# Performance work log

Measured on AMD Instinct MI355X. Metric: run time of the kernel, lower is better.

## Reference

```python
import jax, jax.numpy as jnp
import numpy as np

N, E = 50000, 800000
IN_C, HID_C, OUT_C, HEADS = 128, 32, 16, 4
NEG_SLOPE = 0.2


def gat_conv(x, src, dst, W, att_src, att_dst, bias, heads, out_ch, concat, n_nodes):
    # linear transform: [N, heads, out_ch]
    h = (x @ W).reshape(n_nodes, heads, out_ch)
    # per-node attention logits [N, heads]
    a_s = (h * att_src).sum(-1)
    a_d = (h * att_dst).sum(-1)
    # per-edge raw attention (edge j->i uses src logit of j, dst logit of i)
    alpha = jax.nn.leaky_relu(a_s[src] + a_d[dst], negative_slope=NEG_SLOPE)  # [E, heads]
    # segment softmax over destination neighborhoods
    amax = jax.ops.segment_max(alpha, dst, num_segments=n_nodes)
    ex = jnp.exp(alpha - amax[dst])
    den = jax.ops.segment_sum(ex, dst, num_segments=n_nodes)
    coef = ex / den[dst]  # [E, heads]
    # weighted scatter-add aggregation
    msg = h[src] * coef[:, :, None]  # [E, heads, out_ch]
    out = jax.ops.segment_sum(msg, dst, num_segments=n_nodes)  # [N, heads, out_ch]
    out = out.reshape(n_nodes, heads * out_ch) if concat else out.mean(axis=1)
    return out + bias


def setup_inputs() -> dict:
    key = jax.random.key(0)
    ks = jax.random.split(key, 10)
    x = jax.random.normal(ks[0], (N, IN_C), dtype=jnp.float32)
    edge_index = jax.random.randint(ks[1], (2, E), 0, N, dtype=jnp.int64)
    s1 = 1.0 / np.sqrt(IN_C)
    s2 = 1.0 / np.sqrt(HID_C * HEADS)
    W1 = jax.random.normal(ks[2], (IN_C, HEADS * HID_C), dtype=jnp.float32) * s1
    att_src1 = jax.random.normal(ks[3], (HEADS, HID_C), dtype=jnp.float32) * s1
    att_dst1 = jax.random.normal(ks[4], (HEADS, HID_C), dtype=jnp.float32) * s1
    b1 = jnp.zeros((HEADS * HID_C,), dtype=jnp.float32)
    W2 = jax.random.normal(ks[5], (HEADS * HID_C, OUT_C), dtype=jnp.float32) * s2
    att_src2 = jax.random.normal(ks[6], (1, OUT_C), dtype=jnp.float32) * s2
    att_dst2 = jax.random.normal(ks[7], (1, OUT_C), dtype=jnp.float32) * s2
    b2 = jnp.zeros((OUT_C,), dtype=jnp.float32)
    return {"x": x, "edge_index": edge_index, "W1": W1, "att_src1": att_src1,
            "att_dst1": att_dst1, "b1": b1, "W2": W2, "att_src2": att_src2,
            "att_dst2": att_dst2, "b2": b2}


def reference(x, edge_index, W1, att_src1, att_dst1, b1, W2, att_src2, att_dst2, b2):
    n = x.shape[0]
    # PyG GATConv default: add self loops
    ar = jnp.arange(n, dtype=edge_index.dtype)
    src = jnp.concatenate([edge_index[0], ar])
    dst = jnp.concatenate([edge_index[1], ar])
    h = gat_conv(x, src, dst, W1, att_src1, att_dst1, b1, HEADS, HID_C, True, n)
    h = jax.nn.elu(h)
    out = gat_conv(h, src, dst, W2, att_src2, att_dst2, b2, 1, OUT_C, False, n)
    return out
```

## Files before the change

### kernel.cpp

```cpp
#include <hip/hip_runtime.h>

typedef __attribute__((ext_vector_type(8))) short short8;
typedef __attribute__((ext_vector_type(4))) float f32x4;

__device__ __forceinline__ float lrelu02(float a) { return a > 0.0f ? a : 0.2f * a; }

__device__ __forceinline__ unsigned bf16rne(float f) {
    unsigned u = __float_as_uint(f);
    return (u + 0x7fffu + ((u >> 16) & 1u)) >> 16;
}

__global__ __launch_bounds__(256) void k_zero(int4* __restrict__ p, int n4) {
    int i = blockIdx.x * blockDim.x + threadIdx.x;
    if (i < n4) p[i] = make_int4(0, 0, 0, 0);
}

__global__ __launch_bounds__(256) void k_g1rank(
    const float* __restrict__ x, const float* __restrict__ W,
    const float* __restrict__ attS, const float* __restrict__ attD,
    unsigned short* __restrict__ h1, float* __restrict__ as1, float* __restrict__ ad1,
    const int* __restrict__ ei, int* __restrict__ deg, int* __restrict__ rank,
    int E, int N, int RB)
{
    __shared__ unsigned short Wt[128 * 128];
    __shared__ unsigned short xs[64 * 128];

    if (blockIdx.x < RB) {
        int tid = blockIdx.x * blockDim.x + threadIdx.x;
        int nthr = RB * blockDim.x;
        int E4 = E & ~3;
        for (int b = tid * 4; b < E4; b += nthr * 4) {
            int4 d = *(const int4*)(ei + E + b);
            int4 r;
            r.x = atomicAdd(&deg[d.x], 1);
            r.y = atomicAdd(&deg[d.y], 1);
            r.z = atomicAdd(&deg[d.z], 1);
            r.w = atomicAdd(&deg[d.w], 1);
            *(int4*)(rank + b) = r;
        }
        for (int e = E4 + tid; e < E; e += nthr)
            rank[e] = atomicAdd(&deg[ei[E + e]], 1);
        for (int i = tid; i < N; i += nthr)
            rank[E + i] = atomicAdd(&deg[i], 1);
        return;
    }

    const int t = threadIdx.x;
    const int lane = t & 63;
    const int wv = t >> 6;
    const int ln = lane & 15;
    const int lg = lane >> 4;
    const int r0 = (blockIdx.x - RB) * 64;

    #pragma unroll
    for (int i = 0; i < 16; ++i) {
        int flat = i * 256 + t;
        int n = flat & 127;
        int k0 = (flat >> 7) * 4;
        float v0 = W[(size_t)(k0 + 0) * 128 + n];
        float v1 = W[(size_t)(k0 + 1) * 128 + n];
        float v2 = W[(size_t)(k0 + 2) * 128 + n];
        float v3 = W[(size_t)(k0 + 3) * 128 + n];
        uint2 pk;
        pk.x = bf16rne(v0) | (bf16rne(v1) << 16);
        pk.y = bf16rne(v2) | (bf16rne(v3) << 16);
        int byteo = n * 256 + ((k0 * 2) ^ ((n & 7) << 4));
        *(uint2*)((char*)Wt + byteo) = pk;
    }
    {
        int mbase = t >> 5, k0 = (t & 31) * 4;
        #pragma unroll
        for (int it = 0; it < 8; ++it) {
            int m = mbase + it * 8;
            int rr = r0 + m;
            float4 v = make_float4(0.f, 0.f, 0.f, 0.f);
            if (rr < N) v = *(const float4*)&x[(size_t)rr * 128 + k0];
            unsigned lo = bf16rne(v.x) | (bf16rne(v.y) << 16);
            unsigned hi = bf16rne(v.z) | (bf16rne(v.w) << 16);
            int byteo = m * 256 + ((k0 * 2) ^ ((m & 7) << 4));
            *(uint2*)((char*)xs + byteo) = make_uint2(lo, hi);
        }
    }
    __syncthreads();

    f32x4 acc[8];
    #pragma unroll
    for (int i = 0; i < 8; ++i) acc[i] = (f32x4)(0.f);

    #pragma unroll
    for (int kk = 0; kk < 4; ++kk) {
        int kb = (kk * 32 + lg * 8) * 2;
        int am = wv * 16 + ln;
        short8 a = *(const short8*)((char*)xs + am * 256 + (kb ^ ((am & 7) << 4)));
        #pragma unroll
        for (int tile = 0; tile < 8; ++tile) {
            int n = tile * 16 + ln;
            short8 b = *(const short8*)((char*)Wt + n * 256 + (kb ^ ((n & 7) << 4)));
            acc[tile] = __builtin_amdgcn_mfma_f32_16x16x32_bf16(a, b, acc[tile], 0, 0, 0);
        }
    }

    float aSt[8], aDt[8];
    #pragma unroll
    for (int tile = 0; tile < 8; ++tile) {
        aSt[tile] = attS[tile * 16 + ln];
        aDt[tile] = attD[tile * 16 + ln];
    }
    #pragma unroll
    for (int r = 0; r < 4; ++r) {
        int row = r0 + wv * 16 + lg * 4 + r;
        #pragma unroll
        for (int h = 0; h < 4; ++h) {
            float s = acc[2*h][r] * aSt[2*h] + acc[2*h+1][r] * aSt[2*h+1];
            float d = acc[2*h][r] * aDt[2*h] + acc[2*h+1][r] * aDt[2*h+1];
            s += __shfl_xor(s, 1); s += __shfl_xor(s, 2); s += __shfl_xor(s, 4); s += __shfl_xor(s, 8);
            d += __shfl_xor(d, 1); d += __shfl_xor(d, 2); d += __shfl_xor(d, 4); d += __shfl_xor(d, 8);
            if (ln == h * 4 + r && row < N) {
                as1[row * 4 + h] = s;
                ad1[row * 4 + h] = d;
            }
        }
    }

    __syncthreads();
    #pragma unroll
    for (int tile = 0; tile < 8; ++tile) {
        #pragma unroll
        for (int r = 0; r < 4; ++r) {
            int m = wv * 16 + lg * 4 + r;
            int byteo = m * 256 + (((tile * 16 + ln) * 2) ^ ((m & 7) << 4));
            *(unsigned short*)((char*)xs + byteo) = (unsigned short)bf16rne(acc[tile][r]);
        }
    }
    __syncthreads();
    #pragma unroll
    for (int it = 0; it < 4; ++it) {
        int idx = t + it * 256;
        int m = idx >> 4, o = idx & 15;
        int byteo = m * 256 + ((o * 16) ^ ((m & 7) << 4));
        if (r0 + m < N)
            *(uint4*)((char*)(h1 + (size_t)(r0 + m) * 128) + o * 16) =
                *(const uint4*)((const char*)xs + byteo);
    }
}

__global__ __launch_bounds__(256) void k_scan_local(
    const int* __restrict__ deg, int* __restrict__ rowptr, int* __restrict__ bsum, int N)
{
    const int t = threadIdx.x;
    const int base = blockIdx.x * 2048 + t * 8;
    int v[8];
    int s = 0;
    #pragma unroll
    for (int j = 0; j < 8; ++j) {
        int idx = base + j;
        v[j] = (idx < N) ? deg[idx] : 0;
        s += v[j];
    }
    __shared__ int ts[256];
    ts[t] = s;
    __syncthreads();
    #pragma unroll
    for (int off = 1; off < 256; off <<= 1) {
        int u = (t >= off) ? ts[t - off] : 0;
        __syncthreads();
        ts[t] += u;
        __syncthreads();
    }
    int ex = (t == 0) ? 0 : ts[t - 1];
    #pragma unroll
    for (int j = 0; j < 8; ++j) {
        int idx = base + j;
        if (idx < N) rowptr[idx] = ex;
        ex += v[j];
    }
    if (t == 255) bsum[blockIdx.x] = ts[255];
}

__global__ __launch_bounds__(256) void k_scan_add(
    int* __restrict__ rowptr, const int* __restrict__ bsum, int N, int ET)
{
    const int t = threadIdx.x;
    __shared__ int soff;
    if (t < 64) {
        int v = (t < (int)blockIdx.x) ? bsum[t] : 0;
        #pragma unroll
        for (int m = 32; m >= 1; m >>= 1) v += __shfl_xor(v, m);
        if (t == 0) soff = v;
    }
    __syncthreads();
    int off = soff;
    const int base = blockIdx.x * 2048 + t * 8;
    #pragma unroll
    for (int j = 0; j < 8; ++j) {
        int idx = base + j;
        if (idx < N) rowptr[idx] += off;
    }
    if (blockIdx.x == 0 && t == 0) rowptr[N] = ET;
}

__global__ __launch_bounds__(256) void k_fill2(const int* __restrict__ ei,
                                               const int* __restrict__ rank,
                                               const int* __restrict__ rowptr,
                                               int* __restrict__ col, int E, int N) {
    int tid = blockIdx.x * blockDim.x + threadIdx.x;
    int nthr = gridDim.x * blockDim.x;
    int E4 = E & ~3;
    for (int b = tid * 4; b < E4; b += nthr * 4) {
        int4 d = *(const int4*)(ei + E + b);
        int4 s = *(const int4*)(ei + b);
        int4 r = *(const int4*)(rank + b);
        col[rowptr[d.x] + r.x] = s.x;
        col[rowptr[d.y] + r.y] = s.y;
        col[rowptr[d.z] + r.z] = s.z;
        col[rowptr[d.w] + r.w] = s.w;
    }
    for (int e = E4 + tid; e < E; e += nthr)
        col[rowptr[ei[E + e]] + rank[e]] = ei[e];
    for (int i = tid; i < N; i += nthr)
        col[rowptr[i] + rank[E + i]] = i;
}

__global__ __launch_bounds__(256) void k_agg1(
    const unsigned short* __restrict__ h1, const float* __restrict__ as1,
    const float* __restrict__ ad1, const int* __restrict__ rowptr,
    const int* __restrict__ col, const float* __restrict__ b1,
    unsigned short* __restrict__ out1, int N)
{
    int wid = (int)(((unsigned)blockIdx.x * blockDim.x + threadIdx.x) >> 6);
    if (wid >= N) return;
    int lane = threadIdx.x & 63;
    int start = rowptr[wid], end = rowptr[wid + 1];
    const float4 ad = *(const float4*)(ad1 + (size_t)wid * 4);

    float den0 = 0.f, den1 = 0.f, den2 = 0.f, den3 = 0.f;
    for (int e = start + lane; e < end; e += 64) {
        int src = col[e];
        const float4 a = *(const float4*)(as1 + (size_t)src * 4);
        den0 += __expf(lrelu02(a.x + ad.x));
        den1 += __expf(lrelu02(a.y + ad.y));
        den2 += __expf(lrelu02(a.z + ad.z));
        den3 += __expf(lrelu02(a.w + ad.w));
    }
    #pragma unroll
    for (int m = 32; m >= 1; m >>= 1) {
        den0 += __shfl_xor(den0, m); den1 += __shfl_xor(den1, m);
        den2 += __shfl_xor(den2, m); den3 += __shfl_xor(den3, m);
    }
    int head = lane >> 4;
    float rden = head == 0 ? 1.f/den0 : head == 1 ? 1.f/den1 : head == 2 ? 1.f/den2 : 1.f/den3;
    float adh  = head == 0 ? ad.x : head == 1 ? ad.y : head == 2 ? ad.z : ad.w;

    float acc0 = 0.f, acc1 = 0.f;
    for (int e = start; e < end; e += 8) {
        int s[8];
        float av[8], km[8];
        unsigned hv[8];
        #pragma unroll
        for (int j = 0; j < 8; ++j) {
            int ee = e + j;
            bool ok = ee < end;
            int es = ok ? ee : e;
            s[j]  = col[es];
            km[j] = ok ? 1.f : 0.f;
        }
        #pragma unroll
        for (int j = 0; j < 8; ++j)
            av[j] = as1[(size_t)s[j] * 4 + head];
        #pragma unroll
        for (int j = 0; j < 8; ++j)
            hv[j] = *(const unsigned*)(h1 + (size_t)s[j] * 128 + lane * 2);
        #pragma unroll
        for (int j = 0; j < 8; ++j) {
            float coef = km[j] * __expf(lrelu02(av[j] + adh)) * rden;
            acc0 = fmaf(coef, __uint_as_float(hv[j] << 16), acc0);
            acc1 = fmaf(coef, __uint_as_float(hv[j] & 0xffff0000u), acc1);
        }
    }
    int c0 = lane * 2;
    float o0 = acc0 + b1[c0];
    float o1 = acc1 + b1[c0 + 1];
    o0 = o0 > 0.f ? o0 : expm1f(o0);
    o1 = o1 > 0.f ? o1 : expm1f(o1);
    unsigned ov = bf16rne(o0) | (bf16rne(o1) << 16);
    *(unsigned*)((char*)out1 + (size_t)wid * 256 + lane * 4) = ov;
}

__global__ __launch_bounds__(256) void k_gemm2(
    const unsigned short* __restrict__ in, const float* __restrict__ W,
    const float* __restrict__ attS, const float* __restrict__ attD,
    float* __restrict__ h2, float* __restrict__ as2, float* __restrict__ ad2, int N)
{
    __shared__ unsigned short Wt[16 * 128];
    __shared__ unsigned short xs[64 * 128];
    const int t = threadIdx.x;
    const int lane = t & 63;
    const int wv = t >> 6;
    const int ln = lane & 15;
    const int lg = lane >> 4;
    const int r0 = blockIdx.x * 64;

    #pragma unroll
    for (int i = 0; i < 2; ++i) {
        int flat = i * 256 + t;
        int n = flat & 15;
        int k0 = (flat >> 4) * 4;
        float v0 = W[(size_t)(k0 + 0) * 16 + n];
        float v1 = W[(size_t)(k0 + 1) * 16 + n];
        float v2 = W[(size_t)(k0 + 2) * 16 + n];
        float v3 = W[(size_t)(k0 + 3) * 16 + n];
        uint2 pk;
        pk.x = bf16rne(v0) | (bf16rne(v1) << 16);
        pk.y = bf16rne(v2) | (bf16rne(v3) << 16);
        int byteo = n * 256 + ((k0 * 2) ^ ((n & 7) << 4));
        *(uint2*)((char*)Wt + byteo) = pk;
    }
    #pragma unroll
    for (int it = 0; it < 4; ++it) {
        int idx = t + it * 256;
        int m = idx >> 4, o = idx & 15;
        int rr = r0 + m;
        uint4 v = make_uint4(0, 0, 0, 0);
        if (rr < N) v = *(const uint4*)((const char*)(in + (size_t)rr * 128) + o * 16);
        int byteo = m * 256 + ((o * 16) ^ ((m & 7) << 4));
        *(uint4*)((char*)xs + byteo) = v;
    }
    __syncthreads();

    f32x4 acc = (f32x4)(0.f);
    #pragma unroll
    for (int kk = 0; kk < 4; ++kk) {
        int kb = (kk * 32 + lg * 8) * 2;
        int am = wv * 16 + ln;
        short8 a = *(const short8*)((char*)xs + am * 256 + (kb ^ ((am & 7) << 4)));
        short8 b = *(const short8*)((char*)Wt + ln * 256 + (kb ^ ((ln & 7) << 4)));
        acc = __builtin_amdgcn_mfma_f32_16x16x32_bf16(a, b, acc, 0, 0, 0);
    }

    float aSv = attS[ln], aDv = attD[ln];
    #pragma unroll
    for (int r = 0; r < 4; ++r) {
        int row = r0 + wv * 16 + lg * 4 + r;
        float s = acc[r] * aSv;
        float d = acc[r] * aDv;
        s += __shfl_xor(s, 1); s += __shfl_xor(s, 2); s += __shfl_xor(s, 4); s += __shfl_xor(s, 8);
        d += __shfl_xor(d, 1); d += __shfl_xor(d, 2); d += __shfl_xor(d, 4); d += __shfl_xor(d, 8);
        if (row < N) {
            h2[(size_t)row * 16 + ln] = acc[r];
            if (ln == 0) { as2[row] = s; ad2[row] = d; }
        }
    }
}

__global__ __launch_bounds__(256) void k_agg2(
    const float* __restrict__ h2, const float* __restrict__ as2,
    const float* __restrict__ ad2, const int* __restrict__ rowptr,
    const int* __restrict__ col, const float* __restrict__ b2,
    float* __restrict__ out, int N)
{
    int wid = (int)(((unsigned)blockIdx.x * blockDim.x + threadIdx.x) >> 6);
    if (wid >= N) return;
    int lane = threadIdx.x & 63;
    int start = rowptr[wid], end = rowptr[wid + 1];
    float adv = ad2[wid];

    float den = 0.f;
    for (int e = start + lane; e < end; e += 64)
        den += __expf(lrelu02(as2[col[e]] + adv));
    #pragma unroll
    for (int m = 32; m >= 1; m >>= 1) den += __shfl_xor(den, m);
    float rden = 1.f / den;

    int sub = lane >> 4, c = lane & 15;
    float acc = 0.f;
    for (int e0 = start + sub; e0 < end; e0 += 16) {
        int s[4];
        float av[4], km[4], hvv[4];
        #pragma unroll
        for (int j = 0; j < 4; ++j) {
            int ee = e0 + j * 4;
            bool ok = ee < end;
            int es = ok ? ee : e0;
            s[j]  = col[es];
            km[j] = ok ? 1.f : 0.f;
        }
        #pragma unroll
        for (int j = 0; j < 4; ++j)
            av[j] = as2[s[j]];
        #pragma unroll
        for (int j = 0; j < 4; ++j)
            hvv[j] = h2[(size_t)s[j] * 16 + c];
        #pragma unroll
        for (int j = 0; j < 4; ++j) {
            float coef = km[j] * __expf(lrelu02(av[j] + adv)) * rden;
            acc = fmaf(coef, hvv[j], acc);
        }
    }
    acc += __shfl_xor(acc, 16);
    acc += __shfl_xor(acc, 32);
    if (lane < 16) out[(size_t)wid * 16 + lane] = acc + b2[lane];
}

extern "C" void kernel_launch(void* const* d_in, const int* in_sizes, int n_in,
                              void* d_out, int out_size, void* d_ws, size_t ws_size,
                              hipStream_t stream)
{
    const float* x   = (const float*)d_in[0];
    const int*   ei  = (const int*)d_in[1];
    const float* W1  = (const float*)d_in[2];
    const float* aS1 = (const float*)d_in[3];
    const float* aD1 = (const float*)d_in[4];
    const float* b1  = (const float*)d_in[5];
    const float* W2  = (const float*)d_in[6];
    const float* aS2 = (const float*)d_in[7];
    const float* aD2 = (const float*)d_in[8];
    const float* b2  = (const float*)d_in[9];
    float* out = (float*)d_out;

    int N = in_sizes[0] / 128;
    int E = in_sizes[1] / 2;
    int ET = E + N;
    int nblk = (N + 2047) / 2048;
    int G1 = (N + 63) / 64;
    const int RB = 800;

    char* w = (char*)d_ws;
    auto alloc = [&](size_t bytes) -> void* {
        void* p = (void*)w;
        w += (bytes + 255) & ~(size_t)255;
        return p;
    };
    unsigned short* h1   = (unsigned short*)alloc((size_t)N * 128 * 2);
    unsigned short* out1 = (unsigned short*)alloc((size_t)N * 128 * 2);
    float* as1   = (float*)alloc((size_t)N * 4 * 4);
    float* ad1   = (float*)alloc((size_t)N * 4 * 4);
    float* h2    = (float*)alloc((size_t)N * 16 * 4);
    float* as2v  = (float*)alloc((size_t)N * 4);
    float* ad2v  = (float*)alloc((size_t)N * 4);
    int* deg     = (int*)alloc((size_t)N * 4);
    int* rowptr  = (int*)alloc((size_t)(N + 1) * 4);
    int* rank    = (int*)alloc((size_t)ET * 4);
    int* col     = (int*)alloc((size_t)ET * 4);
    int* bsum    = (int*)alloc(64 * 4);

    const int tb = 256;
    int n4 = (N + 3) / 4;
    k_zero  <<<(n4 + tb - 1) / tb, tb, 0, stream>>>((int4*)deg, n4);
    k_g1rank<<<RB + G1, tb, 0, stream>>>(x, W1, aS1, aD1, h1, as1, ad1,
                                         ei, deg, rank, E, N, RB);
    k_scan_local<<<nblk, tb, 0, stream>>>(deg, rowptr, bsum, N);
    k_scan_add  <<<nblk, tb, 0, stream>>>(rowptr, bsum, N, ET);
    k_fill2     <<<1024, tb, 0, stream>>>(ei, rank, rowptr, col, E, N);

    k_agg1 <<<(N + 3) / 4, tb, 0, stream>>>(h1, as1, ad1, rowptr, col, b1, out1, N);
    k_gemm2<<<G1, tb, 0, stream>>>(out1, W2, aS2, aD2, h2, as2v, ad2v, N);
    k_agg2 <<<(N + 3) / 4, tb, 0, stream>>>(h2, as2v, ad2v, rowptr, col, b2, out, N);
}
```

Baseline: 164.3 us.

## Split degree counters into 8 privatized copies and unfuse rank from GEMM1

The atomic degree counting now spreads over 8 per-class copies of the degree array, chosen by block index, so that atomics on the same destination contend less. The class id is packed into the high bits of the rank. The scan computes per-class offsets and k_fill2 adds them when placing edges. The rank pass is also split out of the fused GEMM1 kernel into its own launch, which removes the overlap between the two. In exchange there is an 8x larger zeroing and scan read, an extra clsoff array, and one more indirect load per edge in fill.

```diff
diff --git a/kernel.cpp b/kernel.cpp
--- a/kernel.cpp
+++ b/kernel.cpp
@@ -15,42 +15,45 @@
     if (i < n4) p[i] = make_int4(0, 0, 0, 0);
 }
 
-__global__ __launch_bounds__(256) void k_g1rank(
+__global__ __launch_bounds__(256) void k_rank(
+    const int* __restrict__ ei, int* __restrict__ deg8, int* __restrict__ rank,
+    int E, int N)
+{
+    const int c = blockIdx.x & 7;
+    int* __restrict__ dc = deg8 + (size_t)c * N;
+    const unsigned cbits = (unsigned)c << 28;
+    int tid = blockIdx.x * blockDim.x + threadIdx.x;
+    int nthr = gridDim.x * blockDim.x;
+    int E4 = E & ~3;
+    for (int b = tid * 4; b < E4; b += nthr * 4) {
+        int4 d = *(const int4*)(ei + E + b);
+        int4 r;
+        r.x = (int)(cbits | (unsigned)atomicAdd(&dc[d.x], 1));
+        r.y = (int)(cbits | (unsigned)atomicAdd(&dc[d.y], 1));
+        r.z = (int)(cbits | (unsigned)atomicAdd(&dc[d.z], 1));
+        r.w = (int)(cbits | (unsigned)atomicAdd(&dc[d.w], 1));
+        *(int4*)(rank + b) = r;
+    }
+    for (int e = E4 + tid; e < E; e += nthr)
+        rank[e] = (int)(cbits | (unsigned)atomicAdd(&dc[ei[E + e]], 1));
+    for (int i = tid; i < N; i += nthr)
+        rank[E + i] = (int)(cbits | (unsigned)atomicAdd(&dc[i], 1));
+}
+
+__global__ __launch_bounds__(256) void k_gemm1(
     const float* __restrict__ x, const float* __restrict__ W,
     const float* __restrict__ attS, const float* __restrict__ attD,
-    unsigned short* __restrict__ h1, float* __restrict__ as1, float* __restrict__ ad1,
-    const int* __restrict__ ei, int* __restrict__ deg, int* __restrict__ rank,
-    int E, int N, int RB)
+    unsigned short* __restrict__ h1, float* __restrict__ as1, float* __restrict__ ad1, int N)
 {
     __shared__ unsigned short Wt[128 * 128];
     __shared__ unsigned short xs[64 * 128];
-
-    if (blockIdx.x < RB) {
-        int tid = blockIdx.x * blockDim.x + threadIdx.x;
-        int nthr = RB * blockDim.x;
-        int E4 = E & ~3;
-        for (int b = tid * 4; b < E4; b += nthr * 4) {
-            int4 d = *(const int4*)(ei + E + b);
-            int4 r;
-            r.x = atomicAdd(&deg[d.x], 1);
-            r.y = atomicAdd(&deg[d.y], 1);
-            r.z = atomicAdd(&deg[d.z], 1);
-            r.w = atomicAdd(&deg[d.w], 1);
-            *(int4*)(rank + b) = r;
-        }
-        for (int e = E4 + tid; e < E; e += nthr)
-            rank[e] = atomicAdd(&deg[ei[E + e]], 1);
-        for (int i = tid; i < N; i += nthr)
-            rank[E + i] = atomicAdd(&deg[i], 1);
-        return;
-    }
 
     const int t = threadIdx.x;
     const int lane = t & 63;
     const int wv = t >> 6;
     const int ln = lane & 15;
     const int lg = lane >> 4;
-    const int r0 = (blockIdx.x - RB) * 64;
+    const int r0 = blockIdx.x * 64;
 
     #pragma unroll
     for (int i = 0; i < 16; ++i) {
@@ -145,18 +148,27 @@
 }
 
 __global__ __launch_bounds__(256) void k_scan_local(
-    const int* __restrict__ deg, int* __restrict__ rowptr, int* __restrict__ bsum, int N)
+    const int* __restrict__ deg8, int* __restrict__ clsoff,
+    int* __restrict__ rowptr, int* __restrict__ bsum, int N)
 {
     const int t = threadIdx.x;
     const int base = blockIdx.x * 2048 + t * 8;
-    int v[8];
+    int v[8] = {0, 0, 0, 0, 0, 0, 0, 0};
+    #pragma unroll
+    for (int c = 0; c < 8; ++c) {
+        #pragma unroll
+        for (int j = 0; j < 8; ++j) {
+            int idx = base + j;
+            if (idx < N) {
+                int dv = deg8[(size_t)c * N + idx];
+                clsoff[(size_t)c * N + idx] = v[j];
+                v[j] += dv;
+            }
+        }
+    }
     int s = 0;
     #pragma unroll
-    for (int j = 0; j < 8; ++j) {
-        int idx = base + j;
-        v[j] = (idx < N) ? deg[idx] : 0;
-        s += v[j];
-    }
+    for (int j = 0; j < 8; ++j) s += v[j];
     __shared__ int ts[256];
     ts[t] = s;
     __syncthreads();
@@ -201,6 +213,7 @@
 
 __global__ __launch_bounds__(256) void k_fill2(const int* __restrict__ ei,
                                                const int* __restrict__ rank,
+                                               const int* __restrict__ clsoff,
                                                const int* __restrict__ rowptr,
                                                int* __restrict__ col, int E, int N) {
     int tid = blockIdx.x * blockDim.x + threadIdx.x;
@@ -210,15 +223,20 @@
         int4 d = *(const int4*)(ei + E + b);
         int4 s = *(const int4*)(ei + b);
         int4 r = *(const int4*)(rank + b);
-        col[rowptr[d.x] + r.x] = s.x;
-        col[rowptr[d.y] + r.y] = s.y;
-        col[rowptr[d.z] + r.z] = s.z;
-        col[rowptr[d.w] + r.w] = s.w;
-    }
-    for (int e = E4 + tid; e < E; e += nthr)
-        col[rowptr[ei[E + e]] + rank[e]] = ei[e];
-    for (int i = tid; i < N; i += nthr)
-        col[rowptr[i] + rank[E + i]] = i;
+        col[rowptr[d.x] + clsoff[(size_t)((unsigned)r.x >> 28) * N + d.x] + (r.x & 0x0FFFFFFF)] = s.x;
+        col[rowptr[d.y] + clsoff[(size_t)((unsigned)r.y >> 28) * N + d.y] + (r.y & 0x0FFFFFFF)] = s.y;
+        col[rowptr[d.z] + clsoff[(size_t)((unsigned)r.z >> 28) * N + d.z] + (r.z & 0x0FFFFFFF)] = s.z;
+        col[rowptr[d.w] + clsoff[(size_t)((unsigned)r.w >> 28) * N + d.w] + (r.w & 0x0FFFFFFF)] = s.w;
+    }
+    for (int e = E4 + tid; e < E; e += nthr) {
+        int d = ei[E + e];
+        int r = rank[e];
+        col[rowptr[d] + clsoff[(size_t)((unsigned)r >> 28) * N + d] + (r & 0x0FFFFFFF)] = ei[e];
+    }
+    for (int i = tid; i < N; i += nthr) {
+        int r = rank[E + i];
+        col[rowptr[i] + clsoff[(size_t)((unsigned)r >> 28) * N + i] + (r & 0x0FFFFFFF)] = i;
+    }
 }
 
 __global__ __launch_bounds__(256) void k_agg1(
@@ -422,7 +440,6 @@
     int ET = E + N;
     int nblk = (N + 2047) / 2048;
     int G1 = (N + 63) / 64;
-    const int RB = 800;
 
     char* w = (char*)d_ws;
     auto alloc = [&](size_t bytes) -> void* {
@@ -437,20 +454,21 @@
     float* h2    = (float*)alloc((size_t)N * 16 * 4);
     float* as2v  = (float*)alloc((size_t)N * 4);
     float* ad2v  = (float*)alloc((size_t)N * 4);
-    int* deg     = (int*)alloc((size_t)N * 4);
+    int* deg8    = (int*)alloc((size_t)N * 8 * 4);
+    int* clsoff  = (int*)alloc((size_t)N * 8 * 4);
     int* rowptr  = (int*)alloc((size_t)(N + 1) * 4);
     int* rank    = (int*)alloc((size_t)ET * 4);
     int* col     = (int*)alloc((size_t)ET * 4);
     int* bsum    = (int*)alloc(64 * 4);
 
     const int tb = 256;
-    int n4 = (N + 3) / 4;
-    k_zero  <<<(n4 + tb - 1) / tb, tb, 0, stream>>>((int4*)deg, n4);
-    k_g1rank<<<RB + G1, tb, 0, stream>>>(x, W1, aS1, aD1, h1, as1, ad1,
-                                         ei, deg, rank, E, N, RB);
-    k_scan_local<<<nblk, tb, 0, stream>>>(deg, rowptr, bsum, N);
+    int n4 = (N * 8 + 3) / 4;
+    k_zero  <<<(n4 + tb - 1) / tb, tb, 0, stream>>>((int4*)deg8, n4);
+    k_rank  <<<2048, tb, 0, stream>>>(ei, deg8, rank, E, N);
+    k_gemm1 <<<G1, tb, 0, stream>>>(x, W1, aS1, aD1, h1, as1, ad1, N);
+    k_scan_local<<<nblk, tb, 0, stream>>>(deg8, clsoff, rowptr, bsum, N);
     k_scan_add  <<<nblk, tb, 0, stream>>>(rowptr, bsum, N, ET);
-    k_fill2     <<<1024, tb, 0, stream>>>(ei, rank, rowptr, col, E, N);
+    k_fill2     <<<1024, tb, 0, stream>>>(ei, rank, clsoff, rowptr, col, E, N);
 
     k_agg1 <<<(N + 3) / 4, tb, 0, stream>>>(h1, as1, ad1, rowptr, col, b1, out1, N);
     k_gemm2<<<G1, tb, 0, stream>>>(out1, W2, aS2, aD2, h2, as2v, ad2v, N);
```

Result: slower. 178.8 us (+8.9%).

## Cache per-edge softmax numerators in registers for low-degree nodes; split rank/gemm kernels

Applied to the files above, without the earlier changes.

For nodes with in-degree of 64 or less, both aggregation kernels now compute each edge's exponentiated logit once, keep it in a register, and broadcast it with shuffles. This replaces the second pass that re-gathered the source logits and recomputed the exponentials. It also splits the fused rank-plus-GEMM1 launch into two separate kernels. That gives up the overlap between the atomic degree counting and the GEMM in exchange for simpler kernels with separate register and LDS footprints.

```diff
diff --git a/kernel.cpp b/kernel.cpp
--- a/kernel.cpp
+++ b/kernel.cpp
@@ -15,42 +15,42 @@
     if (i < n4) p[i] = make_int4(0, 0, 0, 0);
 }
 
-__global__ __launch_bounds__(256) void k_g1rank(
+__global__ __launch_bounds__(256) void k_rank(
+    const int* __restrict__ ei, int* __restrict__ deg, int* __restrict__ rank,
+    int E, int N)
+{
+    int tid = blockIdx.x * blockDim.x + threadIdx.x;
+    int nthr = gridDim.x * blockDim.x;
+    int E4 = E & ~3;
+    for (int b = tid * 4; b < E4; b += nthr * 4) {
+        int4 d = *(const int4*)(ei + E + b);
+        int4 r;
+        r.x = atomicAdd(&deg[d.x], 1);
+        r.y = atomicAdd(&deg[d.y], 1);
+        r.z = atomicAdd(&deg[d.z], 1);
+        r.w = atomicAdd(&deg[d.w], 1);
+        *(int4*)(rank + b) = r;
+    }
+    for (int e = E4 + tid; e < E; e += nthr)
+        rank[e] = atomicAdd(&deg[ei[E + e]], 1);
+    for (int i = tid; i < N; i += nthr)
+        rank[E + i] = atomicAdd(&deg[i], 1);
+}
+
+__global__ __launch_bounds__(256) void k_gemm1(
     const float* __restrict__ x, const float* __restrict__ W,
     const float* __restrict__ attS, const float* __restrict__ attD,
-    unsigned short* __restrict__ h1, float* __restrict__ as1, float* __restrict__ ad1,
-    const int* __restrict__ ei, int* __restrict__ deg, int* __restrict__ rank,
-    int E, int N, int RB)
+    unsigned short* __restrict__ h1, float* __restrict__ as1, float* __restrict__ ad1, int N)
 {
     __shared__ unsigned short Wt[128 * 128];
     __shared__ unsigned short xs[64 * 128];
-
-    if (blockIdx.x < RB) {
-        int tid = blockIdx.x * blockDim.x + threadIdx.x;
-        int nthr = RB * blockDim.x;
-        int E4 = E & ~3;
-        for (int b = tid * 4; b < E4; b += nthr * 4) {
-            int4 d = *(const int4*)(ei + E + b);
-            int4 r;
-            r.x = atomicAdd(&deg[d.x], 1);
-            r.y = atomicAdd(&deg[d.y], 1);
-            r.z = atomicAdd(&deg[d.z], 1);
-            r.w = atomicAdd(&deg[d.w], 1);
-            *(int4*)(rank + b) = r;
-        }
-        for (int e = E4 + tid; e < E; e += nthr)
-            rank[e] = atomicAdd(&deg[ei[E + e]], 1);
-        for (int i = tid; i < N; i += nthr)
-            rank[E + i] = atomicAdd(&deg[i], 1);
-        return;
-    }
 
     const int t = threadIdx.x;
     const int lane = t & 63;
     const int wv = t >> 6;
     const int ln = lane & 15;
     const int lg = lane >> 4;
-    const int r0 = (blockIdx.x - RB) * 64;
+    const int r0 = blockIdx.x * 64;
 
     #pragma unroll
     for (int i = 0; i < 16; ++i) {
@@ -231,52 +231,93 @@
     if (wid >= N) return;
     int lane = threadIdx.x & 63;
     int start = rowptr[wid], end = rowptr[wid + 1];
+    int deg = end - start;
     const float4 ad = *(const float4*)(ad1 + (size_t)wid * 4);
-
-    float den0 = 0.f, den1 = 0.f, den2 = 0.f, den3 = 0.f;
-    for (int e = start + lane; e < end; e += 64) {
-        int src = col[e];
-        const float4 a = *(const float4*)(as1 + (size_t)src * 4);
-        den0 += __expf(lrelu02(a.x + ad.x));
-        den1 += __expf(lrelu02(a.y + ad.y));
-        den2 += __expf(lrelu02(a.z + ad.z));
-        den3 += __expf(lrelu02(a.w + ad.w));
-    }
-    #pragma unroll
-    for (int m = 32; m >= 1; m >>= 1) {
-        den0 += __shfl_xor(den0, m); den1 += __shfl_xor(den1, m);
-        den2 += __shfl_xor(den2, m); den3 += __shfl_xor(den3, m);
-    }
     int head = lane >> 4;
-    float rden = head == 0 ? 1.f/den0 : head == 1 ? 1.f/den1 : head == 2 ? 1.f/den2 : 1.f/den3;
-    float adh  = head == 0 ? ad.x : head == 1 ? ad.y : head == 2 ? ad.z : ad.w;
+    float adh = head == 0 ? ad.x : head == 1 ? ad.y : head == 2 ? ad.z : ad.w;
 
     float acc0 = 0.f, acc1 = 0.f;
-    for (int e = start; e < end; e += 8) {
-        int s[8];
-        float av[8], km[8];
-        unsigned hv[8];
-        #pragma unroll
-        for (int j = 0; j < 8; ++j) {
-            int ee = e + j;
-            bool ok = ee < end;
-            int es = ok ? ee : e;
-            s[j]  = col[es];
-            km[j] = ok ? 1.f : 0.f;
-        }
-        #pragma unroll
-        for (int j = 0; j < 8; ++j)
-            av[j] = as1[(size_t)s[j] * 4 + head];
-        #pragma unroll
-        for (int j = 0; j < 8; ++j)
-            hv[j] = *(const unsigned*)(h1 + (size_t)s[j] * 128 + lane * 2);
-        #pragma unroll
-        for (int j = 0; j < 8; ++j) {
-            float coef = km[j] * __expf(lrelu02(av[j] + adh)) * rden;
-            acc0 = fmaf(coef, __uint_as_float(hv[j] << 16), acc0);
-            acc1 = fmaf(coef, __uint_as_float(hv[j] & 0xffff0000u), acc1);
-        }
-    }
+
+    if (deg <= 64) {
+        int idx = lane & 15;
+        float ex[4];
+        float den = 0.f;
+        #pragma unroll
+        for (int b = 0; b < 4; ++b) {
+            int j = b * 16 + idx;
+            float v = 0.f;
+            if (j < deg) {
+                int src = col[start + j];
+                v = __expf(lrelu02(as1[(size_t)src * 4 + head] + adh));
+            }
+            ex[b] = v;
+            den += v;
+        }
+        den += __shfl_xor(den, 1); den += __shfl_xor(den, 2);
+        den += __shfl_xor(den, 4); den += __shfl_xor(den, 8);
+        float rden = 1.f / den;
+        int srcbase = lane & 48;
+        #pragma unroll
+        for (int b = 0; b < 4; ++b) {
+            if (b * 16 >= deg) break;
+            int s[16]; float cf[16]; unsigned hv[16];
+            #pragma unroll
+            for (int q = 0; q < 16; ++q) {
+                int j = b * 16 + q;
+                s[q]  = col[start + (j < deg ? j : 0)];
+                cf[q] = __shfl(ex[b], srcbase | q);
+            }
+            #pragma unroll
+            for (int q = 0; q < 16; ++q)
+                hv[q] = *(const unsigned*)(h1 + (size_t)s[q] * 128 + lane * 2);
+            #pragma unroll
+            for (int q = 0; q < 16; ++q) {
+                float coef = cf[q] * rden;
+                acc0 = fmaf(coef, __uint_as_float(hv[q] << 16), acc0);
+                acc1 = fmaf(coef, __uint_as_float(hv[q] & 0xffff0000u), acc1);
+            }
+        }
+    } else {
+        float den0 = 0.f, den1 = 0.f, den2 = 0.f, den3 = 0.f;
+        for (int e = start + lane; e < end; e += 64) {
+            int src = col[e];
+            const float4 a = *(const float4*)(as1 + (size_t)src * 4);
+            den0 += __expf(lrelu02(a.x + ad.x));
+            den1 += __expf(lrelu02(a.y + ad.y));
+            den2 += __expf(lrelu02(a.z + ad.z));
+            den3 += __expf(lrelu02(a.w + ad.w));
+        }
+        #pragma unroll
+        for (int m = 32; m >= 1; m >>= 1) {
+            den0 += __shfl_xor(den0, m); den1 += __shfl_xor(den1, m);
+            den2 += __shfl_xor(den2, m); den3 += __shfl_xor(den3, m);
+        }
+        float rden = head == 0 ? 1.f/den0 : head == 1 ? 1.f/den1 : head == 2 ? 1.f/den2 : 1.f/den3;
+        for (int e = start; e < end; e += 8) {
+            int s[8]; float av[8], km[8]; unsigned hv[8];
+            #pragma unroll
+            for (int j = 0; j < 8; ++j) {
+                int ee = e + j;
+                bool ok = ee < end;
+                int es = ok ? ee : e;
+                s[j]  = col[es];
+                km[j] = ok ? 1.f : 0.f;
+            }
+            #pragma unroll
+            for (int j = 0; j < 8; ++j)
+                av[j] = as1[(size_t)s[j] * 4 + head];
+            #pragma unroll
+            for (int j = 0; j < 8; ++j)
+                hv[j] = *(const unsigned*)(h1 + (size_t)s[j] * 128 + lane * 2);
+            #pragma unroll
+            for (int j = 0; j < 8; ++j) {
+                float coef = km[j] * __expf(lrelu02(av[j] + adh)) * rden;
+                acc0 = fmaf(coef, __uint_as_float(hv[j] << 16), acc0);
+                acc1 = fmaf(coef, __uint_as_float(hv[j] & 0xffff0000u), acc1);
+            }
+        }
+    }
+
     int c0 = lane * 2;
     float o0 = acc0 + b1[c0];
     float o1 = acc1 + b1[c0 + 1];
@@ -362,40 +403,66 @@
     if (wid >= N) return;
     int lane = threadIdx.x & 63;
     int start = rowptr[wid], end = rowptr[wid + 1];
+    int deg = end - start;
     float adv = ad2[wid];
-
-    float den = 0.f;
-    for (int e = start + lane; e < end; e += 64)
-        den += __expf(lrelu02(as2[col[e]] + adv));
-    #pragma unroll
-    for (int m = 32; m >= 1; m >>= 1) den += __shfl_xor(den, m);
-    float rden = 1.f / den;
-
     int sub = lane >> 4, c = lane & 15;
     float acc = 0.f;
-    for (int e0 = start + sub; e0 < end; e0 += 16) {
-        int s[4];
-        float av[4], km[4], hvv[4];
-        #pragma unroll
-        for (int j = 0; j < 4; ++j) {
-            int ee = e0 + j * 4;
-            bool ok = ee < end;
-            int es = ok ? ee : e0;
-            s[j]  = col[es];
-            km[j] = ok ? 1.f : 0.f;
-        }
-        #pragma unroll
-        for (int j = 0; j < 4; ++j)
-            av[j] = as2[s[j]];
-        #pragma unroll
-        for (int j = 0; j < 4; ++j)
-            hvv[j] = h2[(size_t)s[j] * 16 + c];
-        #pragma unroll
-        for (int j = 0; j < 4; ++j) {
-            float coef = km[j] * __expf(lrelu02(av[j] + adv)) * rden;
-            acc = fmaf(coef, hvv[j], acc);
-        }
-    }
+
+    if (deg <= 64) {
+        float ex0 = 0.f;
+        if (lane < deg) ex0 = __expf(lrelu02(as2[col[start + lane]] + adv));
+        float den = ex0;
+        #pragma unroll
+        for (int m = 32; m >= 1; m >>= 1) den += __shfl_xor(den, m);
+        float rden = 1.f / den;
+        #pragma unroll
+        for (int g = 0; g < 4; ++g) {
+            if (g * 16 >= deg) break;
+            int s[4]; float cf[4], hv[4];
+            #pragma unroll
+            for (int jj = 0; jj < 4; ++jj) {
+                int j = g * 16 + jj * 4 + sub;
+                s[jj]  = col[start + (j < deg ? j : 0)];
+                cf[jj] = __shfl(ex0, j);
+            }
+            #pragma unroll
+            for (int jj = 0; jj < 4; ++jj)
+                hv[jj] = h2[(size_t)s[jj] * 16 + c];
+            #pragma unroll
+            for (int jj = 0; jj < 4; ++jj)
+                acc = fmaf(cf[jj] * rden, hv[jj], acc);
+        }
+    } else {
+        float den = 0.f;
+        for (int e = start + lane; e < end; e += 64)
+            den += __expf(lrelu02(as2[col[e]] + adv));
+        #pragma unroll
+        for (int m = 32; m >= 1; m >>= 1) den += __shfl_xor(den, m);
+        float rden = 1.f / den;
+        for (int e0 = start + sub; e0 < end; e0 += 16) {
+            int s[4]; float av[4], km[4], hv[4];
+            #pragma unroll
+            for (int jj = 0; jj < 4; ++jj) {
+                int ee = e0 + jj * 4;
+                bool ok = ee < end;
+                int es = ok ? ee : e0;
+                s[jj]  = col[es];
+                km[jj] = ok ? 1.f : 0.f;
+            }
+            #pragma unroll
+            for (int jj = 0; jj < 4; ++jj)
+                av[jj] = as2[s[jj]];
+            #pragma unroll
+            for (int jj = 0; jj < 4; ++jj)
+                hv[jj] = h2[(size_t)s[jj] * 16 + c];
+            #pragma unroll
+            for (int jj = 0; jj < 4; ++jj) {
+                float coef = km[jj] * __expf(lrelu02(av[jj] + adv)) * rden;
+                acc = fmaf(coef, hv[jj], acc);
+            }
+        }
+    }
+
     acc += __shfl_xor(acc, 16);
     acc += __shfl_xor(acc, 32);
     if (lane < 16) out[(size_t)wid * 16 + lane] = acc + b2[lane];
@@ -422,7 +489,6 @@
     int ET = E + N;
     int nblk = (N + 2047) / 2048;
     int G1 = (N + 63) / 64;
-    const int RB = 800;
 
     char* w = (char*)d_ws;
     auto alloc = [&](size_t bytes) -> void* {
@@ -446,8 +512,8 @@
     const int tb = 256;
     int n4 = (N + 3) / 4;
     k_zero  <<<(n4 + tb - 1) / tb, tb, 0, stream>>>((int4*)deg, n4);
-    k_g1rank<<<RB + G1, tb, 0, stream>>>(x, W1, aS1, aD1, h1, as1, ad1,
-                                         ei, deg, rank, E, N, RB);
+    k_rank  <<<2048, tb, 0, stream>>>(ei, deg, rank, E, N);
+    k_gemm1 <<<G1, tb, 0, stream>>>(x, W1, aS1, aD1, h1, as1, ad1, N);
     k_scan_local<<<nblk, tb, 0, stream>>>(deg, rowptr, bsum, N);
     k_scan_add  <<<nblk, tb, 0, stream>>>(rowptr, bsum, N, ET);
     k_fill2     <<<1024, tb, 0, stream>>>(ei, rank, rowptr, col, E, N);
```

New measurement: 164.8 us. Within noise of the previous version (+0.3%).
